# Kernel tuning notes

Measured on AMD Instinct MI355X. Metric: run time of the kernel, lower is better.

The kernel has to match this reference:

```python
import jax, jax.numpy as jnp
import numpy as np

B, T, C, H, L, V = 8, 512, 512, 8, 2, 512
DH = C // H
SCALE = 1.0 / np.sqrt(DH)


def _ln(x, g, b):
    mu = jnp.mean(x, -1, keepdims=True)
    var = jnp.mean((x - mu) ** 2, -1, keepdims=True)
    return (x - mu) * jax.lax.rsqrt(var + 1e-5) * g + b


def setup_inputs() -> dict:
    key = jax.random.key(0)
    ks = jax.random.split(key, 16)
    f = lambda k, shape: jax.random.normal(k, shape, jnp.float32) * 0.02
    return {
        "idx": jax.random.randint(ks[0], (B, T), 0, 4),
        "tok_emb": f(ks[1], (4, C)),
        "pos_emb": f(ks[2], (T, C)),
        "ln1_g": jnp.ones((L, C)), "ln1_b": jnp.zeros((L, C)),
        "Wq": f(ks[3], (L, C, C)), "bq": jnp.zeros((L, C)),
        "Wk": f(ks[4], (L, C, C)), "bk": jnp.zeros((L, C)),
        "Wv": f(ks[5], (L, C, C)), "bv": jnp.zeros((L, C)),
        "Wp": f(ks[6], (L, C, C)), "bp": jnp.zeros((L, C)),
        "ln2_g": jnp.ones((L, C)), "ln2_b": jnp.zeros((L, C)),
        "W1": f(ks[7], (L, C, 4 * C)), "b1": jnp.zeros((L, 4 * C)),
        "W2": f(ks[8], (L, 4 * C, C)), "b2": jnp.zeros((L, C)),
        "lnf_g": jnp.ones((C,)), "lnf_b": jnp.zeros((C,)),
        "Whead": f(ks[9], (C, V)),
        "steps": 4,
    }


def _block(x, p):
    (l1g, l1b, wq, bq, wk, bk, wv, bv, wp, bp,
     l2g, l2b, w1, b1, w2, b2) = p
    # attention (mask buffer is all ones in the original -> full attention)
    xn = _ln(x, l1g, l1b)
    q = (xn @ wq + bq).reshape(B, T, H, DH)
    k = (xn @ wk + bk).reshape(B, T, H, DH)
    v = (xn @ wv + bv).reshape(B, T, H, DH)
    att = jnp.einsum('bqhd,bkhd->bhqk', q, k) * SCALE
    att = jax.nn.softmax(att, axis=-1)
    y = jnp.einsum('bhqk,bkhd->bqhd', att, v).reshape(B, T, C)
    x = x + y @ wp + bp
    # MLP with exact (erf) GELU, matching torch nn.GELU default
    h = jax.nn.gelu(_ln(x, l2g, l2b) @ w1 + b1, approximate=False)
    return x + h @ w2 + b2


def reference(idx, tok_emb, pos_emb, ln1_g, ln1_b, Wq, bq, Wk, bk, Wv, bv,
              Wp, bp, ln2_g, ln2_b, W1, b1, W2, b2, lnf_g, lnf_b, Whead,
              steps):
    params = (ln1_g, ln1_b, Wq, bq, Wk, bk, Wv, bv, Wp, bp,
              ln2_g, ln2_b, W1, b1, W2, b2)
    x = tok_emb[idx] + pos_emb[None, :, :]

    def run_blocks(x):
        def step(x, p):
            return _block(x, p), None
        x, _ = jax.lax.scan(step, x, params)
        return x

    for _ in range(steps):  # recurrent application of the whole stack
        x = run_blocks(x)
    x = _ln(x, lnf_g, lnf_b)
    return x @ Whead  # logits [B, T, V]
```

## Files before the change

### kernel.cpp

```cpp
#include <hip/hip_runtime.h>
#include <hip/hip_bf16.h>
#include <math.h>

#define BB 8
#define TT 512
#define CC 512
#define HH 8
#define DH 64
#define LL 2
#define VV 512
#define NSTEPS 4
#define BT (BB*TT)
#define FF (4*CC)

typedef unsigned short u16;
typedef __bf16 bf16x8 __attribute__((ext_vector_type(8)));
typedef float f32x4 __attribute__((ext_vector_type(4)));
typedef u16 u16x8 __attribute__((ext_vector_type(8)));

static __device__ __forceinline__ u16 f2bf(float f) {
    unsigned int u = __float_as_uint(f);
    unsigned int r = (u + 0x7fffu + ((u >> 16) & 1u)) >> 16;
    return (u16)r;
}

static __device__ __forceinline__ void async16(const void* g, void* l) {
    __builtin_amdgcn_global_load_lds((__attribute__((address_space(1))) void*)g,
                                     (__attribute__((address_space(3))) void*)l, 16, 0, 0);
}

static __device__ __forceinline__ int swzp(int r) { return (r ^ (r >> 2)) & 7; }

__global__ __launch_bounds__(256)
void ln_kernel(const float* __restrict__ x, const float* __restrict__ g,
               const float* __restrict__ b, u16* __restrict__ out) {
    int wid = threadIdx.x >> 6, lane = threadIdx.x & 63;
    int row = blockIdx.x * 4 + wid;
    const float* xr = x + (size_t)row * CC;
    f32x4 v0 = ((const f32x4*)xr)[lane*2];
    f32x4 v1 = ((const f32x4*)xr)[lane*2 + 1];
    float s = 0.f, sq = 0.f;
#pragma unroll
    for (int j = 0; j < 4; j++) {
        s += v0[j] + v1[j];
        sq += v0[j]*v0[j] + v1[j]*v1[j];
    }
#pragma unroll
    for (int off = 1; off < 64; off <<= 1) { s += __shfl_xor(s, off); sq += __shfl_xor(sq, off); }
    float mean = s * (1.0f / CC);
    float var  = sq * (1.0f / CC) - mean * mean;
    float inv  = rsqrtf(var + 1e-5f);
    f32x4 g0 = ((const f32x4*)g)[lane*2], g1 = ((const f32x4*)g)[lane*2 + 1];
    f32x4 b0 = ((const f32x4*)b)[lane*2], b1 = ((const f32x4*)b)[lane*2 + 1];
    u16x8 o;
#pragma unroll
    for (int j = 0; j < 4; j++) o[j]     = f2bf((v0[j] - mean) * inv * g0[j] + b0[j]);
#pragma unroll
    for (int j = 0; j < 4; j++) o[4 + j] = f2bf((v1[j] - mean) * inv * g1[j] + b1[j]);
    *(u16x8*)&out[(size_t)row*CC + lane*8] = o;
}

__global__ __launch_bounds__(256)
void prologue_kernel(const float* __restrict__ Wq, const float* __restrict__ Wk,
                     const float* __restrict__ Wv, const float* __restrict__ Wp,
                     const float* __restrict__ W1, const float* __restrict__ W2,
                     const float* __restrict__ Wh,
                     u16* w_qkvt, u16* w_pt, u16* w_1t, u16* w_2t, u16* w_ht,
                     const int* __restrict__ idx, const float* __restrict__ tok,
                     const float* __restrict__ pos, float* __restrict__ x) {
    int bid = blockIdx.x;
    if (bid >= 1600) {
        int bt = bid - 1600;
        int t  = threadIdx.x;
        int token = idx[bt];
        int posrow = bt % TT;
        x[(size_t)bt*CC + t]       = tok[token*CC + t]       + pos[posrow*CC + t];
        x[(size_t)bt*CC + t + 256] = tok[token*CC + t + 256] + pos[posrow*CC + t + 256];
        return;
    }
    const float* src; u16* dst; int K, N, i0, j0;
    const size_t wcc = (size_t)CC*CC, wcf = (size_t)CC*FF;
    if (bid < 1536) {
        int l = bid / 768, r = bid % 768;
        if (r < 256) {
            int m = r / 64, t = r % 64;
            K = CC; N = CC;
            i0 = (t / 8) * 64; j0 = (t % 8) * 64;
            if      (m == 0) { src = Wq + l*wcc; dst = w_qkvt + (size_t)l*3*wcc; }
            else if (m == 1) { src = Wk + l*wcc; dst = w_qkvt + (size_t)l*3*wcc + wcc; }
            else if (m == 2) { src = Wv + l*wcc; dst = w_qkvt + (size_t)l*3*wcc + 2*wcc; }
            else             { src = Wp + l*wcc; dst = w_pt + (size_t)l*wcc; }
        } else if (r < 512) {
            int t = r - 256;
            K = CC; N = FF;
            i0 = (t / 32) * 64; j0 = (t % 32) * 64;
            src = W1 + l*wcf; dst = w_1t + (size_t)l*wcf;
        } else {
            int t = r - 512;
            K = FF; N = CC;
            i0 = (t / 8) * 64; j0 = (t % 8) * 64;
            src = W2 + l*wcf; dst = w_2t + (size_t)l*wcf;
        }
    } else {
        int t = bid - 1536;
        K = CC; N = CC;
        i0 = (t / 8) * 64; j0 = (t % 8) * 64;
        src = Wh; dst = w_ht;
    }
    __shared__ float tile[64][65];
    int tt = threadIdx.x;
    int rr = tt >> 2, cg = (tt & 3) * 16;
#pragma unroll
    for (int i = 0; i < 16; i++)
        tile[rr][cg + i] = src[(size_t)(i0 + rr) * N + j0 + cg + i];
    __syncthreads();
#pragma unroll
    for (int i = 0; i < 16; i++)
        dst[(size_t)(j0 + rr) * K + i0 + cg + i] = f2bf(tile[cg + i][rr]);
}

template<int BM, int BN, int THREADS, int WROWS, int WCOLS, int EPI>
__global__ __launch_bounds__(THREADS, 6)
void gemm_bt_kernel(const u16* __restrict__ A, const u16* __restrict__ Bt,
                    int N, int K,
                    const float* __restrict__ bias, const float* __restrict__ biask,
                    const float* __restrict__ biasv,
                    float* outf, u16* outq, u16* outk, u16* outvt) {
    constexpr int WTM = BM / WROWS, WTN = BN / WCOLS;
    constexpr int TM = WTM / 16, TN = WTN / 16;
    static_assert(THREADS / 4 == 2 * BM, "A staged in exactly one call");
    static_assert(THREADS == WROWS * WCOLS * 64, "wave grid");
    __shared__ u16 lds_a[2][2][BM][32];
    __shared__ u16 lds_b[2][2][BN][32];
    int tid = threadIdx.x;
    int wid = tid >> 6, lane = tid & 63;
    int quad = lane >> 4, l15 = lane & 15;
    int wm = (wid % WROWS) * WTM, wn = (wid / WROWS) * WTN;

    int NBN = N / BN;
    int lin = blockIdx.x;
    int x8 = lin & 7, slot = lin >> 3;
    int bn = slot % NBN;
    int bm = (slot / NBN) * 8 + x8;

    const int fr = tid >> 2;
    const int c2 = tid & 3;
    const size_t a0 = (size_t)bm * BM, b0 = (size_t)bn * BN;

    auto stage = [&](int buf, int kt) {
        {
            int ks2 = fr / BM, row = fr % BM;
            int g = (ks2 * 4 + c2) ^ swzp(row);
            async16(&A[(a0 + row) * K + kt + g * 8], &lds_a[buf][ks2][row][c2 * 8]);
        }
#pragma unroll
        for (int i = 0; i < (2 * BN) / (THREADS / 4); i++) {
            int f = fr + i * (THREADS / 4);
            int ks2 = f / BN, row = f % BN;
            int g = (ks2 * 4 + c2) ^ swzp(row);
            async16(&Bt[(b0 + row) * K + kt + g * 8], &lds_b[buf][ks2][row][c2 * 8]);
        }
    };

    f32x4 zero = {0.f, 0.f, 0.f, 0.f};
    f32x4 acc[TM][TN];
#pragma unroll
    for (int mi = 0; mi < TM; mi++)
#pragma unroll
        for (int ni = 0; ni < TN; ni++) acc[mi][ni] = zero;

    stage(0, 0);
    __syncthreads();
    const int NKT = K / 64;
    for (int kt = 0; kt < NKT; kt++) {
        int cur = kt & 1;
        if (kt + 1 < NKT) stage(cur ^ 1, (kt + 1) * 64);
#pragma unroll
        for (int ks = 0; ks < 2; ks++) {
            bf16x8 af[TM], bfr[TN];
#pragma unroll
            for (int mi = 0; mi < TM; mi++) {
                int row = wm + mi*16 + l15;
                int lc = (ks*4 + quad) ^ swzp(row);
                af[mi] = *(const bf16x8*)&lds_a[cur][lc >> 2][row][(lc & 3) * 8];
            }
#pragma unroll
            for (int ni = 0; ni < TN; ni++) {
                int row = wn + ni*16 + l15;
                int lc = (ks*4 + quad) ^ swzp(row);
                bfr[ni] = *(const bf16x8*)&lds_b[cur][lc >> 2][row][(lc & 3) * 8];
            }
#pragma unroll
            for (int mi = 0; mi < TM; mi++)
#pragma unroll
                for (int ni = 0; ni < TN; ni++)
                    acc[mi][ni] = __builtin_amdgcn_mfma_f32_16x16x32_bf16(af[mi], bfr[ni], acc[mi][ni], 0, 0, 0);
        }
        __syncthreads();
    }

#pragma unroll
    for (int mi = 0; mi < TM; mi++)
#pragma unroll
        for (int ni = 0; ni < TN; ni++)
#pragma unroll
            for (int i = 0; i < 4; i++) {
                int row = bm*BM + wm + mi*16 + quad*4 + i;
                int col = bn*BN + wn + ni*16 + l15;
                float v = acc[mi][ni][i];
                if (EPI == 0) {
                    int region = col >> 9, cl = col & 511;
                    if (region == 0) {
                        v = (v + bias[cl]) * 0.125f;
                        outq[(size_t)row*512 + cl] = f2bf(v);
                    } else if (region == 1) {
                        v += biask[cl];
                        outk[(size_t)row*512 + cl] = f2bf(v);
                    } else {
                        v += biasv[cl];
                        int bb = row >> 9, tpos = row & 511, hh = cl >> 6, dh = cl & 63;
                        outvt[(((size_t)(bb*8 + hh)*64 + dh) << 9) + tpos] = f2bf(v);
                    }
                } else if (EPI == 1) {
                    size_t idx2 = (size_t)row * N + col;
                    v += bias[col] + outf[idx2];
                    outf[idx2] = v;
                } else if (EPI == 2) {
                    v += bias[col];
                    v = 0.5f * v * (1.0f + erff(v * 0.70710678118654752f));
                    outq[(size_t)row * N + col] = f2bf(v);
                } else {
                    outf[(size_t)row * N + col] = v;
                }
            }
}

__global__ __launch_bounds__(256)
void attn_mfma_kernel(const u16* __restrict__ q, const u16* __restrict__ k,
                      const u16* __restrict__ vt, u16* __restrict__ y) {
    __shared__ u16 lq[64][64];
    __shared__ u16 lk[2][64][64];
    __shared__ u16 lv[2][64][64];
    __shared__ u16 lp[4][16][72];
    int qt = blockIdx.x, h = blockIdx.y, b = blockIdx.z;
    int tid = threadIdx.x;
    int wid = tid >> 6, lane = tid & 63;
    int quad = lane >> 4, l15 = lane & 15;
    const int sr = tid >> 3;
    const int sc = (tid & 7) * 8;
    const int gsc = (((tid & 7) ^ swzp(sr)) << 3);

    auto stageKV = [&](int buf, int kt) {
#pragma unroll
        for (int c = 0; c < 2; c++) {
            async16(&k[(size_t)(b*TT + kt*64 + c*32 + sr)*CC + h*DH + gsc], &lk[buf][c*32 + sr][sc]);
            async16(&vt[((size_t)((b*HH + h)*DH + c*32 + sr))*TT + kt*64 + gsc], &lv[buf][c*32 + sr][sc]);
        }
    };

#pragma unroll
    for (int c = 0; c < 2; c++)
        async16(&q[(size_t)(b*TT + qt*64 + c*32 + sr)*CC + h*DH + gsc], &lq[c*32 + sr][sc]);
    stageKV(0, 0);
    __syncthreads();

    f32x4 zero = {0.f, 0.f, 0.f, 0.f};
    f32x4 acc_o[4];
    float m_st[4], l_st[4];
#pragma unroll
    for (int i = 0; i < 4; i++) { m_st[i] = -INFINITY; l_st[i] = 0.f; }
#pragma unroll
    for (int ni = 0; ni < 4; ni++) acc_o[ni] = zero;

    const int rowq = wid*16 + l15;
    const int pq = swzp(rowq);

    for (int kt = 0; kt < TT/64; kt++) {
        int cur = kt & 1;
        if (kt + 1 < TT/64) stageKV(cur ^ 1, kt + 1);

        f32x4 s[4];
#pragma unroll
        for (int ni = 0; ni < 4; ni++) s[ni] = zero;
#pragma unroll
        for (int ks = 0; ks < 2; ks++) {
            int lcq = (ks*4 + quad) ^ pq;
            bf16x8 aq = *(const bf16x8*)&lq[rowq][lcq * 8];
            bf16x8 bfr[4];
#pragma unroll
            for (int ni = 0; ni < 4; ni++) {
                int rowk = ni*16 + l15;
                int lck = (ks*4 + quad) ^ swzp(rowk);
                bfr[ni] = *(const bf16x8*)&lk[cur][rowk][lck * 8];
            }
#pragma unroll
            for (int ni = 0; ni < 4; ni++)
                s[ni] = __builtin_amdgcn_mfma_f32_16x16x32_bf16(aq, bfr[ni], s[ni], 0, 0, 0);
        }

#pragma unroll
        for (int i = 0; i < 4; i++) {
            float mx = -INFINITY;
#pragma unroll
            for (int ni = 0; ni < 4; ni++) mx = fmaxf(mx, s[ni][i]);
#pragma unroll
            for (int off = 1; off < 16; off <<= 1) mx = fmaxf(mx, __shfl_xor(mx, off));
            float mn = fmaxf(m_st[i], mx);
            float al = __expf(m_st[i] - mn);
            float rs = 0.f;
#pragma unroll
            for (int ni = 0; ni < 4; ni++) {
                float p = __expf(s[ni][i] - mn);
                s[ni][i] = p;
                rs += p;
            }
#pragma unroll
            for (int off = 1; off < 16; off <<= 1) rs += __shfl_xor(rs, off);
            l_st[i] = l_st[i] * al + rs;
            m_st[i] = mn;
#pragma unroll
            for (int ni = 0; ni < 4; ni++) acc_o[ni][i] *= al;
        }

#pragma unroll
        for (int ni = 0; ni < 4; ni++)
#pragma unroll
            for (int i = 0; i < 4; i++)
                lp[wid][quad*4 + i][ni*16 + l15] = f2bf(s[ni][i]);

#pragma unroll
        for (int ks = 0; ks < 2; ks++) {
            bf16x8 pa = *(const bf16x8*)&lp[wid][l15][ks*32 + quad*8];
            bf16x8 vb[4];
#pragma unroll
            for (int ni = 0; ni < 4; ni++) {
                int rowv = ni*16 + l15;
                int lcv = (ks*4 + quad) ^ swzp(rowv);
                vb[ni] = *(const bf16x8*)&lv[cur][rowv][lcv * 8];
            }
#pragma unroll
            for (int ni = 0; ni < 4; ni++)
                acc_o[ni] = __builtin_amdgcn_mfma_f32_16x16x32_bf16(pa, vb[ni], acc_o[ni], 0, 0, 0);
        }
        __syncthreads();
    }

#pragma unroll
    for (int i = 0; i < 4; i++) {
        float inv = 1.0f / l_st[i];
#pragma unroll
        for (int ni = 0; ni < 4; ni++) {
            int qrow = qt*64 + wid*16 + quad*4 + i;
            int col  = h*DH + ni*16 + l15;
            y[(size_t)(b*TT + qrow)*CC + col] = f2bf(acc_o[ni][i] * inv);
        }
    }
}

extern "C" void kernel_launch(void* const* d_in, const int* in_sizes, int n_in,
                              void* d_out, int out_size, void* d_ws, size_t ws_size,
                              hipStream_t stream) {
    const int*   idx   = (const int*)d_in[0];
    const float* tok   = (const float*)d_in[1];
    const float* pos   = (const float*)d_in[2];
    const float* ln1g  = (const float*)d_in[3];
    const float* ln1b  = (const float*)d_in[4];
    const float* Wq    = (const float*)d_in[5];
    const float* bq    = (const float*)d_in[6];
    const float* Wk    = (const float*)d_in[7];
    const float* bk    = (const float*)d_in[8];
    const float* Wv    = (const float*)d_in[9];
    const float* bv    = (const float*)d_in[10];
    const float* Wp    = (const float*)d_in[11];
    const float* bp    = (const float*)d_in[12];
    const float* ln2g  = (const float*)d_in[13];
    const float* ln2b  = (const float*)d_in[14];
    const float* W1    = (const float*)d_in[15];
    const float* b1    = (const float*)d_in[16];
    const float* W2    = (const float*)d_in[17];
    const float* b2    = (const float*)d_in[18];
    const float* lnfg  = (const float*)d_in[19];
    const float* lnfb  = (const float*)d_in[20];
    const float* Whead = (const float*)d_in[21];

    float* x  = (float*)d_ws;
    u16* xn   = (u16*)(x + (size_t)BT*CC);
    u16* R    = xn + (size_t)BT*CC;
    u16* qb   = R;
    u16* kb   = R + (size_t)BT*CC;
    u16* vtb  = R + (size_t)2*BT*CC;
    u16* hb   = R;
    u16* w_qkvt = R + (size_t)4*BT*CC;
    u16* w_pt   = w_qkvt + (size_t)2*3*CC*CC;
    u16* w_1t   = w_pt   + (size_t)2*CC*CC;
    u16* w_2t   = w_1t   + (size_t)2*CC*FF;
    u16* w_ht   = w_2t   + (size_t)2*FF*CC;

    prologue_kernel<<<1600 + BT, 256, 0, stream>>>(Wq, Wk, Wv, Wp, W1, W2, Whead,
                                                   w_qkvt, w_pt, w_1t, w_2t, w_ht,
                                                   idx, tok, pos, x);

    const int g_qkv  = (3*CC/128) * (BT/64);
    const int g_fc1  = (FF/128)   * (BT/64);
    const int g_proj = (CC/64)    * (BT/32);
    const int g_fc2  = (CC/64)    * (BT/32);
    const int g_head = (VV/64)    * (BT/32);

    for (int s = 0; s < NSTEPS; s++) {
        for (int l = 0; l < LL; l++) {
            ln_kernel<<<BT/4, 256, 0, stream>>>(x, ln1g + l*CC, ln1b + l*CC, xn);
            gemm_bt_kernel<64,128,512,2,4,0><<<g_qkv, 512, 0, stream>>>(
                xn, w_qkvt + (size_t)l*3*CC*CC, 3*CC, CC,
                bq + l*CC, bk + l*CC, bv + l*CC, nullptr, qb, kb, vtb);
            attn_mfma_kernel<<<dim3(TT/64, HH, BB), 256, 0, stream>>>(qb, kb, vtb, xn);
            gemm_bt_kernel<32,64,256,2,2,1><<<g_proj, 256, 0, stream>>>(
                xn, w_pt + (size_t)l*CC*CC, CC, CC,
                bp + l*CC, nullptr, nullptr, x, nullptr, nullptr, nullptr);
            ln_kernel<<<BT/4, 256, 0, stream>>>(x, ln2g + l*CC, ln2b + l*CC, xn);
            gemm_bt_kernel<64,128,512,2,4,2><<<g_fc1, 512, 0, stream>>>(
                xn, w_1t + (size_t)l*CC*FF, FF, CC,
                b1 + (size_t)l*FF, nullptr, nullptr, nullptr, hb, nullptr, nullptr);
            gemm_bt_kernel<32,64,256,2,2,1><<<g_fc2, 256, 0, stream>>>(
                hb, w_2t + (size_t)l*FF*CC, CC, FF,
                b2 + l*CC, nullptr, nullptr, x, nullptr, nullptr, nullptr);
        }
    }

    ln_kernel<<<BT/4, 256, 0, stream>>>(x, lnfg, lnfb, xn);
    gemm_bt_kernel<32,64,256,2,2,3><<<g_head, 256, 0, stream>>>(
        xn, w_ht, VV, CC, nullptr, nullptr, nullptr, (float*)d_out, nullptr, nullptr, nullptr);
}
```

Baseline: 917.6 us.

## Fold LayerNorm into GEMMs via weight scaling and epilogue row statistics

```diff
diff --git a/kernel.cpp b/kernel.cpp
--- a/kernel.cpp
+++ b/kernel.cpp
@@ -32,69 +32,83 @@
 static __device__ __forceinline__ int swzp(int r) { return (r ^ (r >> 2)) & 7; }
 
 __global__ __launch_bounds__(256)
-void ln_kernel(const float* __restrict__ x, const float* __restrict__ g,
-               const float* __restrict__ b, u16* __restrict__ out) {
-    int wid = threadIdx.x >> 6, lane = threadIdx.x & 63;
-    int row = blockIdx.x * 4 + wid;
-    const float* xr = x + (size_t)row * CC;
-    f32x4 v0 = ((const f32x4*)xr)[lane*2];
-    f32x4 v1 = ((const f32x4*)xr)[lane*2 + 1];
-    float s = 0.f, sq = 0.f;
-#pragma unroll
-    for (int j = 0; j < 4; j++) {
-        s += v0[j] + v1[j];
-        sq += v0[j]*v0[j] + v1[j]*v1[j];
-    }
-#pragma unroll
-    for (int off = 1; off < 64; off <<= 1) { s += __shfl_xor(s, off); sq += __shfl_xor(sq, off); }
-    float mean = s * (1.0f / CC);
-    float var  = sq * (1.0f / CC) - mean * mean;
-    float inv  = rsqrtf(var + 1e-5f);
-    f32x4 g0 = ((const f32x4*)g)[lane*2], g1 = ((const f32x4*)g)[lane*2 + 1];
-    f32x4 b0 = ((const f32x4*)b)[lane*2], b1 = ((const f32x4*)b)[lane*2 + 1];
-    u16x8 o;
-#pragma unroll
-    for (int j = 0; j < 4; j++) o[j]     = f2bf((v0[j] - mean) * inv * g0[j] + b0[j]);
-#pragma unroll
-    for (int j = 0; j < 4; j++) o[4 + j] = f2bf((v1[j] - mean) * inv * g1[j] + b1[j]);
-    *(u16x8*)&out[(size_t)row*CC + lane*8] = o;
-}
-
-__global__ __launch_bounds__(256)
 void prologue_kernel(const float* __restrict__ Wq, const float* __restrict__ Wk,
                      const float* __restrict__ Wv, const float* __restrict__ Wp,
                      const float* __restrict__ W1, const float* __restrict__ W2,
                      const float* __restrict__ Wh,
+                     const float* __restrict__ ln1g, const float* __restrict__ ln1b,
+                     const float* __restrict__ ln2g, const float* __restrict__ ln2b,
+                     const float* __restrict__ lnfg, const float* __restrict__ lnfb,
                      u16* w_qkvt, u16* w_pt, u16* w_1t, u16* w_2t, u16* w_ht,
                      const int* __restrict__ idx, const float* __restrict__ tok,
-                     const float* __restrict__ pos, float* __restrict__ x) {
+                     const float* __restrict__ pos, float* __restrict__ x,
+                     u16* __restrict__ xb, float* __restrict__ ucb,
+                     float2* __restrict__ sp) {
     int bid = blockIdx.x;
-    if (bid >= 1600) {
-        int bt = bid - 1600;
+    const size_t wcc = (size_t)CC*CC, wcf = (size_t)CC*FF;
+    if (bid >= 1630) {
+        int bt = bid - 1630;
         int t  = threadIdx.x;
         int token = idx[bt];
-        int posrow = bt % TT;
-        x[(size_t)bt*CC + t]       = tok[token*CC + t]       + pos[posrow*CC + t];
-        x[(size_t)bt*CC + t + 256] = tok[token*CC + t + 256] + pos[posrow*CC + t + 256];
+        int posrow = bt & (TT - 1);
+        float v0 = tok[token*CC + t]       + pos[posrow*CC + t];
+        float v1 = tok[token*CC + t + 256] + pos[posrow*CC + t + 256];
+        size_t base = (size_t)bt*CC;
+        x[base + t] = v0;            x[base + t + 256] = v1;
+        xb[base + t] = f2bf(v0);     xb[base + t + 256] = f2bf(v1);
+        float s = v0 + v1, q = v0*v0 + v1*v1;
+#pragma unroll
+        for (int off = 1; off < 64; off <<= 1) { s += __shfl_xor(s, off); q += __shfl_xor(q, off); }
+        __shared__ float rs[4], rq[4];
+        int wid = t >> 6, lane = t & 63;
+        if (lane == 0) { rs[wid] = s; rq[wid] = q; }
+        __syncthreads();
+        if (t == 0)      sp[(size_t)bt*8] = make_float2(rs[0]+rs[1]+rs[2]+rs[3],
+                                                        rq[0]+rq[1]+rq[2]+rq[3]);
+        else if (t < 8)  sp[(size_t)bt*8 + t] = make_float2(0.f, 0.f);
         return;
     }
-    const float* src; u16* dst; int K, N, i0, j0;
-    const size_t wcc = (size_t)CC*CC, wcf = (size_t)CC*FF;
+    if (bid >= 1600) {
+        int c = (bid - 1600)*256 + threadIdx.x;
+        const float* Wsrc; const float* gv; const float* bv2; float* up; float* cp;
+        int n, Nd;
+        if (c < 3072) {
+            int l = c / 1536, w = c % 1536, m = w / 512; n = w % 512; Nd = CC;
+            Wsrc = (m == 0 ? Wq : (m == 1 ? Wk : Wv)) + l*wcc;
+            gv = ln1g + l*CC; bv2 = ln1b + l*CC;
+            up = ucb + c; cp = ucb + 3072 + c;
+        } else if (c < 7168) {
+            int d = c - 3072, l = d / 2048; n = d % 2048; Nd = FF;
+            Wsrc = W1 + l*wcf; gv = ln2g + l*CC; bv2 = ln2b + l*CC;
+            up = ucb + 6144 + d; cp = ucb + 10240 + d;
+        } else {
+            n = c - 7168; Nd = VV; Wsrc = Wh; gv = lnfg; bv2 = lnfb;
+            up = ucb + 14336 + n; cp = ucb + 14848 + n;
+        }
+        float su = 0.f, sc = 0.f;
+        for (int k = 0; k < CC; k++) {
+            float w = Wsrc[(size_t)k*Nd + n];
+            su += gv[k]*w; sc += bv2[k]*w;
+        }
+        *up = su; *cp = sc;
+        return;
+    }
+    const float* src; u16* dst; const float* gv = nullptr; int K, N, i0, j0;
     if (bid < 1536) {
         int l = bid / 768, r = bid % 768;
         if (r < 256) {
             int m = r / 64, t = r % 64;
             K = CC; N = CC;
             i0 = (t / 8) * 64; j0 = (t % 8) * 64;
-            if      (m == 0) { src = Wq + l*wcc; dst = w_qkvt + (size_t)l*3*wcc; }
-            else if (m == 1) { src = Wk + l*wcc; dst = w_qkvt + (size_t)l*3*wcc + wcc; }
-            else if (m == 2) { src = Wv + l*wcc; dst = w_qkvt + (size_t)l*3*wcc + 2*wcc; }
+            if      (m == 0) { src = Wq + l*wcc; dst = w_qkvt + (size_t)l*3*wcc;          gv = ln1g + l*CC; }
+            else if (m == 1) { src = Wk + l*wcc; dst = w_qkvt + (size_t)l*3*wcc + wcc;    gv = ln1g + l*CC; }
+            else if (m == 2) { src = Wv + l*wcc; dst = w_qkvt + (size_t)l*3*wcc + 2*wcc;  gv = ln1g + l*CC; }
             else             { src = Wp + l*wcc; dst = w_pt + (size_t)l*wcc; }
         } else if (r < 512) {
             int t = r - 256;
             K = CC; N = FF;
             i0 = (t / 32) * 64; j0 = (t % 32) * 64;
-            src = W1 + l*wcf; dst = w_1t + (size_t)l*wcf;
+            src = W1 + l*wcf; dst = w_1t + (size_t)l*wcf; gv = ln2g + l*CC;
         } else {
             int t = r - 512;
             K = FF; N = CC;
@@ -105,14 +119,15 @@
         int t = bid - 1536;
         K = CC; N = CC;
         i0 = (t / 8) * 64; j0 = (t % 8) * 64;
-        src = Wh; dst = w_ht;
+        src = Wh; dst = w_ht; gv = lnfg;
     }
     __shared__ float tile[64][65];
     int tt = threadIdx.x;
     int rr = tt >> 2, cg = (tt & 3) * 16;
+    float gk = gv ? gv[i0 + rr] : 1.0f;
 #pragma unroll
     for (int i = 0; i < 16; i++)
-        tile[rr][cg + i] = src[(size_t)(i0 + rr) * N + j0 + cg + i];
+        tile[rr][cg + i] = src[(size_t)(i0 + rr) * N + j0 + cg + i] * gk;
     __syncthreads();
 #pragma unroll
     for (int i = 0; i < 16; i++)
@@ -120,18 +135,24 @@
 }
 
 template<int BM, int BN, int THREADS, int WROWS, int WCOLS, int EPI>
-__global__ __launch_bounds__(THREADS, 6)
+__global__ __launch_bounds__(THREADS, 4)
 void gemm_bt_kernel(const u16* __restrict__ A, const u16* __restrict__ Bt,
                     int N, int K,
                     const float* __restrict__ bias, const float* __restrict__ biask,
                     const float* __restrict__ biasv,
+                    const float* __restrict__ uvec, const float* __restrict__ cvec,
+                    const float2* __restrict__ spin, float2* __restrict__ spout,
                     float* outf, u16* outq, u16* outk, u16* outvt) {
     constexpr int WTM = BM / WROWS, WTN = BN / WCOLS;
     constexpr int TM = WTM / 16, TN = WTN / 16;
-    static_assert(THREADS / 4 == 2 * BM, "A staged in exactly one call");
+    constexpr bool FOLD = (EPI == 0 || EPI == 2 || EPI == 3);
     static_assert(THREADS == WROWS * WCOLS * 64, "wave grid");
+    static_assert((8*BM) % THREADS == 0 && (8*BN) % THREADS == 0, "staging divisibility");
+    static_assert(EPI != 1 || (BM == 64 && BN == 128 && WROWS == 2 && WCOLS == 4), "stats layout");
     __shared__ u16 lds_a[2][2][BM][32];
     __shared__ u16 lds_b[2][2][BN][32];
+    __shared__ float s_rs[FOLD ? BM : 1], s_mrs[FOLD ? BM : 1];
+    __shared__ float psum[2][64][2], psq[2][64][2];
     int tid = threadIdx.x;
     int wid = tid >> 6, lane = tid & 63;
     int quad = lane >> 4, l15 = lane & 15;
@@ -143,22 +164,24 @@
     int bn = slot % NBN;
     int bm = (slot / NBN) * 8 + x8;
 
-    const int fr = tid >> 2;
-    const int c2 = tid & 3;
     const size_t a0 = (size_t)bm * BM, b0 = (size_t)bn * BN;
 
     auto stage = [&](int buf, int kt) {
-        {
-            int ks2 = fr / BM, row = fr % BM;
-            int g = (ks2 * 4 + c2) ^ swzp(row);
-            async16(&A[(a0 + row) * K + kt + g * 8], &lds_a[buf][ks2][row][c2 * 8]);
-        }
-#pragma unroll
-        for (int i = 0; i < (2 * BN) / (THREADS / 4); i++) {
-            int f = fr + i * (THREADS / 4);
-            int ks2 = f / BN, row = f % BN;
-            int g = (ks2 * 4 + c2) ^ swzp(row);
-            async16(&Bt[(b0 + row) * K + kt + g * 8], &lds_b[buf][ks2][row][c2 * 8]);
+#pragma unroll
+        for (int i = 0; i < (8*BM)/THREADS; i++) {
+            int f = tid + i*THREADS;
+            int ks2 = f / (4*BM), rem = f % (4*BM);
+            int row = rem >> 2, c2 = rem & 3;
+            int g = (ks2*4 + c2) ^ swzp(row);
+            async16(&A[(a0 + row)*K + kt + g*8], (u16*)lds_a[buf] + (size_t)f*8);
+        }
+#pragma unroll
+        for (int i = 0; i < (8*BN)/THREADS; i++) {
+            int f = tid + i*THREADS;
+            int ks2 = f / (4*BN), rem = f % (4*BN);
+            int row = rem >> 2, c2 = rem & 3;
+            int g = (ks2*4 + c2) ^ swzp(row);
+            async16(&Bt[(b0 + row)*K + kt + g*8], (u16*)lds_b[buf] + (size_t)f*8);
         }
     };
 
@@ -199,15 +222,40 @@
         __syncthreads();
     }
 
+    if (FOLD) {
+        for (int r = tid; r < BM; r += THREADS) {
+            float s = 0.f, q = 0.f;
+#pragma unroll
+            for (int j = 0; j < 8; j++) { float2 p = spin[(a0 + r)*8 + j]; s += p.x; q += p.y; }
+            float mu  = s * (1.0f / CC);
+            float var = q * (1.0f / CC) - mu * mu;
+            float rstd = rsqrtf(var + 1e-5f);
+            s_rs[r] = rstd; s_mrs[r] = mu * rstd;
+        }
+        __syncthreads();
+    }
+
+    float lsum[TM][4], lsq[TM][4];
+    if (EPI == 1) {
+#pragma unroll
+        for (int mi = 0; mi < TM; mi++)
+#pragma unroll
+            for (int i = 0; i < 4; i++) { lsum[mi][i] = 0.f; lsq[mi][i] = 0.f; }
+    }
+
 #pragma unroll
     for (int mi = 0; mi < TM; mi++)
 #pragma unroll
-        for (int ni = 0; ni < TN; ni++)
+        for (int ni = 0; ni < TN; ni++) {
+            int col = bn*BN + wn + ni*16 + l15;
+            float uc_ = 0.f, cc_ = 0.f;
+            if (FOLD) { uc_ = uvec[col]; cc_ = cvec[col]; }
 #pragma unroll
             for (int i = 0; i < 4; i++) {
-                int row = bm*BM + wm + mi*16 + quad*4 + i;
-                int col = bn*BN + wn + ni*16 + l15;
+                int rloc = wm + mi*16 + quad*4 + i;
+                int row = bm*BM + rloc;
                 float v = acc[mi][ni][i];
+                if (FOLD) v = s_rs[rloc]*v - s_mrs[rloc]*uc_ + cc_;
                 if (EPI == 0) {
                     int region = col >> 9, cl = col & 511;
                     if (region == 0) {
@@ -222,9 +270,11 @@
                         outvt[(((size_t)(bb*8 + hh)*64 + dh) << 9) + tpos] = f2bf(v);
                     }
                 } else if (EPI == 1) {
-                    size_t idx2 = (size_t)row * N + col;
-                    v += bias[col] + outf[idx2];
-                    outf[idx2] = v;
+                    size_t id2 = (size_t)row * N + col;
+                    v += bias[col] + outf[id2];
+                    outf[id2] = v;
+                    outq[id2] = f2bf(v);
+                    lsum[mi][i] += v; lsq[mi][i] += v*v;
                 } else if (EPI == 2) {
                     v += bias[col];
                     v = 0.5f * v * (1.0f + erff(v * 0.70710678118654752f));
@@ -233,6 +283,30 @@
                     outf[(size_t)row * N + col] = v;
                 }
             }
+        }
+
+    if (EPI == 1) {
+        int half = (wn >> 5) & 1, slice = wn >> 6;
+#pragma unroll
+        for (int mi = 0; mi < TM; mi++)
+#pragma unroll
+            for (int i = 0; i < 4; i++) {
+                float s = lsum[mi][i], q = lsq[mi][i];
+#pragma unroll
+                for (int off = 1; off < 16; off <<= 1) { s += __shfl_xor(s, off); q += __shfl_xor(q, off); }
+                if (l15 == 0) {
+                    int pr = wm + mi*16 + quad*4 + i;
+                    psum[slice][pr][half] = s; psq[slice][pr][half] = q;
+                }
+            }
+        __syncthreads();
+        if (tid < 2*BM) {
+            int pr = tid >> 1, s2 = tid & 1;
+            spout[(a0 + pr)*8 + bn*2 + s2] =
+                make_float2(psum[s2][pr][0] + psum[s2][pr][1],
+                            psq[s2][pr][0] + psq[s2][pr][1]);
+        }
+    }
 }
 
 __global__ __launch_bounds__(256)
@@ -384,8 +458,9 @@
     const float* Whead = (const float*)d_in[21];
 
     float* x  = (float*)d_ws;
-    u16* xn   = (u16*)(x + (size_t)BT*CC);
-    u16* R    = xn + (size_t)BT*CC;
+    u16* xb   = (u16*)(x + (size_t)BT*CC);
+    u16* yb   = xb + (size_t)BT*CC;
+    u16* R    = yb + (size_t)BT*CC;
     u16* qb   = R;
     u16* kb   = R + (size_t)BT*CC;
     u16* vtb  = R + (size_t)2*BT*CC;
@@ -395,38 +470,47 @@
     u16* w_1t   = w_pt   + (size_t)2*CC*CC;
     u16* w_2t   = w_1t   + (size_t)2*CC*FF;
     u16* w_ht   = w_2t   + (size_t)2*FF*CC;
-
-    prologue_kernel<<<1600 + BT, 256, 0, stream>>>(Wq, Wk, Wv, Wp, W1, W2, Whead,
+    float* ucb  = (float*)(w_ht + (size_t)CC*VV);
+    float2* sp  = (float2*)(ucb + 15360);
+
+    prologue_kernel<<<1630 + BT, 256, 0, stream>>>(Wq, Wk, Wv, Wp, W1, W2, Whead,
+                                                   ln1g, ln1b, ln2g, ln2b, lnfg, lnfb,
                                                    w_qkvt, w_pt, w_1t, w_2t, w_ht,
-                                                   idx, tok, pos, x);
-
-    const int g_qkv  = (3*CC/128) * (BT/64);
-    const int g_fc1  = (FF/128)   * (BT/64);
-    const int g_proj = (CC/64)    * (BT/32);
-    const int g_fc2  = (CC/64)    * (BT/32);
-    const int g_head = (VV/64)    * (BT/32);
+                                                   idx, tok, pos, x, xb, ucb, sp);
+
+    const int g_qkv = (3*CC/128) * (BT/128);
+    const int g_fc1 = (FF/128)   * (BT/128);
+    const int g_pf  = (CC/128)   * (BT/64);
 
     for (int s = 0; s < NSTEPS; s++) {
         for (int l = 0; l < LL; l++) {
-            ln_kernel<<<BT/4, 256, 0, stream>>>(x, ln1g + l*CC, ln1b + l*CC, xn);
-            gemm_bt_kernel<64,128,512,2,4,0><<<g_qkv, 512, 0, stream>>>(
-                xn, w_qkvt + (size_t)l*3*CC*CC, 3*CC, CC,
-                bq + l*CC, bk + l*CC, bv + l*CC, nullptr, qb, kb, vtb);
-            attn_mfma_kernel<<<dim3(TT/64, HH, BB), 256, 0, stream>>>(qb, kb, vtb, xn);
-            gemm_bt_kernel<32,64,256,2,2,1><<<g_proj, 256, 0, stream>>>(
-                xn, w_pt + (size_t)l*CC*CC, CC, CC,
-                bp + l*CC, nullptr, nullptr, x, nullptr, nullptr, nullptr);
-            ln_kernel<<<BT/4, 256, 0, stream>>>(x, ln2g + l*CC, ln2b + l*CC, xn);
-            gemm_bt_kernel<64,128,512,2,4,2><<<g_fc1, 512, 0, stream>>>(
-                xn, w_1t + (size_t)l*CC*FF, FF, CC,
-                b1 + (size_t)l*FF, nullptr, nullptr, nullptr, hb, nullptr, nullptr);
-            gemm_bt_kernel<32,64,256,2,2,1><<<g_fc2, 256, 0, stream>>>(
+            gemm_bt_kernel<128,128,512,2,4,0><<<g_qkv, 512, 0, stream>>>(
+                xb, w_qkvt + (size_t)l*3*CC*CC, 3*CC, CC,
+                bq + l*CC, bk + l*CC, bv + l*CC,
+                ucb + l*1536, ucb + 3072 + l*1536, sp, nullptr,
+                nullptr, qb, kb, vtb);
+            attn_mfma_kernel<<<dim3(TT/64, HH, BB), 256, 0, stream>>>(qb, kb, vtb, yb);
+            gemm_bt_kernel<64,128,512,2,4,1><<<g_pf, 512, 0, stream>>>(
+                yb, w_pt + (size_t)l*CC*CC, CC, CC,
+                bp + l*CC, nullptr, nullptr,
+                nullptr, nullptr, nullptr, sp,
+                x, xb, nullptr, nullptr);
+            gemm_bt_kernel<128,128,512,2,4,2><<<g_fc1, 512, 0, stream>>>(
+                xb, w_1t + (size_t)l*CC*FF, FF, CC,
+                b1 + (size_t)l*FF, nullptr, nullptr,
+                ucb + 6144 + l*2048, ucb + 10240 + l*2048, sp, nullptr,
+                nullptr, hb, nullptr, nullptr);
+            gemm_bt_kernel<64,128,512,2,4,1><<<g_pf, 512, 0, stream>>>(
                 hb, w_2t + (size_t)l*FF*CC, CC, FF,
-                b2 + l*CC, nullptr, nullptr, x, nullptr, nullptr, nullptr);
-        }
-    }
-
-    ln_kernel<<<BT/4, 256, 0, stream>>>(x, lnfg, lnfb, xn);
-    gemm_bt_kernel<32,64,256,2,2,3><<<g_head, 256, 0, stream>>>(
-        xn, w_ht, VV, CC, nullptr, nullptr, nullptr, (float*)d_out, nullptr, nullptr, nullptr);
+                b2 + l*CC, nullptr, nullptr,
+                nullptr, nullptr, nullptr, sp,
+                x, xb, nullptr, nullptr);
+        }
+    }
+
+    gemm_bt_kernel<64,128,512,2,4,3><<<g_pf, 512, 0, stream>>>(
+        xb, w_ht, VV, CC,
+        nullptr, nullptr, nullptr,
+        ucb + 14336, ucb + 14848, sp, nullptr,
+        (float*)d_out, nullptr, nullptr, nullptr);
 }
```

New measurement: 1.051 ms. 1.15x slower.
